# Optimization experiments

Measured on AMD Instinct MI355X. Metric: run time of the kernel, lower is better.

## Reference

```python
import jax, jax.numpy as jnp
import numpy as np

N_NODES = 50000
N_EDGES = 800000
IN_DIM = 128
HIDDEN = 128
CLASSES = 64


def setup_inputs() -> dict:
    key = jax.random.key(0)
    ks = jax.random.split(key, 10)
    features = jax.random.normal(ks[0], (N_NODES, IN_DIM), dtype=jnp.float32)
    W1 = jax.random.normal(ks[1], (HIDDEN, IN_DIM), dtype=jnp.float32) * (2.0 / np.sqrt(IN_DIM + HIDDEN))
    b1 = jnp.zeros((HIDDEN,), dtype=jnp.float32)
    W2 = jax.random.normal(ks[2], (CLASSES, HIDDEN), dtype=jnp.float32) * (2.0 / np.sqrt(HIDDEN + CLASSES))
    b2 = jnp.zeros((CLASSES,), dtype=jnp.float32)
    order_attn = jax.random.uniform(ks[3], (2,), dtype=jnp.float32)
    src1 = jax.random.randint(ks[4], (N_EDGES,), 0, N_NODES, dtype=jnp.int32)
    dst1 = jax.random.randint(ks[5], (N_EDGES,), 0, N_NODES, dtype=jnp.int32)
    src2 = jax.random.randint(ks[6], (N_EDGES,), 0, N_NODES, dtype=jnp.int32)
    dst2 = jax.random.randint(ks[7], (N_EDGES,), 0, N_NODES, dtype=jnp.int32)
    return {"features": features, "W1": W1, "b1": b1, "W2": W2, "b2": b2,
            "order_attn": order_attn, "src1": src1, "dst1": dst1,
            "src2": src2, "dst2": dst2}


def _gin_conv(x, src, dst, W, b):
    # DGL GINConv, aggregator_type='sum', eps=0 (default, non-learnable):
    # h_v = Linear( x_v + sum_{(u->v) in E} x_u )
    agg = jax.ops.segment_sum(x[src], dst, num_segments=N_NODES)  # [N, D]
    return (x + agg) @ W.T + b


def reference(features, W1, b1, W2, b2, order_attn, src1, dst1, src2, dst2):
    a0, a1 = order_attn[0], order_attn[1]
    # layer 1 over both order-graphs
    x11 = jax.nn.elu(a0 * _gin_conv(features, src1, dst1, W1, b1))
    x12 = jax.nn.elu(a1 * _gin_conv(features, src2, dst2, W1, b1))
    x1 = x11 + x12  # [N, hidden]
    # layer 2 over both order-graphs
    x21 = jax.nn.elu(a0 * _gin_conv(x1, src1, dst1, W2, b2))
    x22 = jax.nn.elu(a1 * _gin_conv(x1, src2, dst2, W2, b2))
    return x21 + x22  # [N, classes]
```

## Files before the change

kernel.cpp:

```cpp
#include <hip/hip_runtime.h>
#include <math.h>

#define N_NODES 50000
#define N_EDGES 800000
#define IN_DIM 128
#define HIDDEN 128
#define CLASSES 64
#define N2 100000

#define BIN_SHIFT 8
#define BIN_SZ 256
#define NB 391
#define NBLK 256
#define CHUNK ((2 * N_EDGES + NBLK - 1) / NBLK)

#define NSTRIP 3125
#define GBLK 391

typedef __attribute__((ext_vector_type(8))) short bf16x8;
typedef __attribute__((ext_vector_type(4))) float f32x4;

union FragU {
    uint4 u4;
    uint2 u2[2];
    bf16x8 f;
};

static __device__ __forceinline__ float elu_f(float x) {
    return x > 0.f ? x : (expf(x) - 1.f);
}

static __device__ __forceinline__ unsigned pack_bf2(float a, float b) {
    unsigned ua = __float_as_uint(a);
    ua = (ua + 0x7FFFu + ((ua >> 16) & 1u)) >> 16;
    unsigned ub = __float_as_uint(b);
    ub = (ub + 0x7FFFu + ((ub >> 16) & 1u)) >> 16;
    return ua | (ub << 16);
}

static __device__ __forceinline__ unsigned short bf1(float x) {
    unsigned u = __float_as_uint(x);
    u = (u + 0x7FFFu + ((u >> 16) & 1u)) >> 16;
    return (unsigned short)u;
}

static __device__ __forceinline__ float2 bf2f2(unsigned u) {
    float2 r;
    r.x = __uint_as_float(u << 16);
    r.y = __uint_as_float(u & 0xFFFF0000u);
    return r;
}

static __device__ __forceinline__ void acc4(float4& a, const uint2 u) {
    const float2 lo = bf2f2(u.x);
    const float2 hi = bf2f2(u.y);
    a.x += lo.x; a.y += lo.y; a.z += hi.x; a.w += hi.y;
}

__global__ __launch_bounds__(1024) void k_p1_count(
    const int* __restrict__ dst1, const int* __restrict__ dst2,
    int* __restrict__ counts)
{
    __shared__ int hist[NB];
    const int t = threadIdx.x, b = blockIdx.x;
    if (t < NB) hist[t] = 0;
    __syncthreads();
    const int beg = b * CHUNK;
    const int end = min(beg + CHUNK, 2 * N_EDGES);
    for (int i = beg + t; i < end; i += 1024) {
        const int idx = (i < N_EDGES) ? dst1[i] : (N_NODES + dst2[i - N_EDGES]);
        atomicAdd(&hist[idx >> BIN_SHIFT], 1);
    }
    __syncthreads();
    if (t < NB) counts[t * NBLK + b] = hist[t];
}

__global__ __launch_bounds__(512) void k_scan_bins(
    int* __restrict__ counts, int* __restrict__ binStart, int* __restrict__ off)
{
    __shared__ int tot[512];
    const int t = threadIdx.x;
    int total = 0;
    if (t < NB) {
        const int4* p = reinterpret_cast<const int4*>(counts + t * NBLK);
        #pragma unroll 8
        for (int i = 0; i < NBLK / 4; ++i) {
            const int4 c = p[i];
            total += (c.x + c.y) + (c.z + c.w);
        }
    }
    tot[t] = (t < NB) ? total : 0;
    __syncthreads();
    const int v = tot[t];
    for (int d = 1; d < 512; d <<= 1) {
        const int x = (t >= d) ? tot[t - d] : 0;
        __syncthreads();
        tot[t] += x;
        __syncthreads();
    }
    const int excl = tot[t] - v;
    if (t < NB) binStart[t] = excl;
    if (t == NB - 1) binStart[NB] = tot[t];
    if (t == 0) off[N2] = 2 * N_EDGES;
    if (t < NB) {
        int run = excl;
        int* p = counts + t * NBLK;
        for (int i = 0; i < NBLK; i += 4) {
            int4 c = *reinterpret_cast<int4*>(p + i);
            int4 w;
            w.x = run; run += c.x;
            w.y = run; run += c.y;
            w.z = run; run += c.z;
            w.w = run; run += c.w;
            *reinterpret_cast<int4*>(p + i) = w;
        }
    }
}

__global__ __launch_bounds__(1024) void k_p2_scatter(
    const int* __restrict__ src1, const int* __restrict__ dst1,
    const int* __restrict__ src2, const int* __restrict__ dst2,
    const int* __restrict__ counts, unsigned* __restrict__ binned)
{
    __shared__ int cur[NB];
    const int t = threadIdx.x, b = blockIdx.x;
    if (t < NB) cur[t] = counts[t * NBLK + b];
    __syncthreads();
    const int beg = b * CHUNK;
    const int end = min(beg + CHUNK, 2 * N_EDGES);
    for (int i = beg + t; i < end; i += 1024) {
        int s, idx;
        if (i < N_EDGES) { s = src1[i]; idx = dst1[i]; }
        else             { s = src2[i - N_EDGES]; idx = N_NODES + dst2[i - N_EDGES]; }
        const int bin = idx >> BIN_SHIFT;
        const unsigned rec = ((unsigned)s << BIN_SHIFT) | (unsigned)(idx & (BIN_SZ - 1));
        const int pos = atomicAdd(&cur[bin], 1);
        binned[pos] = rec;
    }
}

__global__ __launch_bounds__(1024) void k_p3_csr(
    const unsigned* __restrict__ binned, const int* __restrict__ binStart,
    int* __restrict__ off, int* __restrict__ csr)
{
    __shared__ int hist[BIN_SZ], sc[BIN_SZ], cur[BIN_SZ];
    const int t = threadIdx.x, bin = blockIdx.x;
    const int bs = binStart[bin], be = binStart[bin + 1];
    const int base = bin << BIN_SHIFT;
    const int nloc = min(BIN_SZ, N2 - base);
    if (t < BIN_SZ) hist[t] = 0;
    __syncthreads();
    for (int p = bs + t; p < be; p += 1024)
        atomicAdd(&hist[binned[p] & (BIN_SZ - 1u)], 1);
    __syncthreads();
    int v = 0;
    if (t < BIN_SZ) { v = hist[t]; sc[t] = v; }
    __syncthreads();
    for (int d = 1; d < BIN_SZ; d <<= 1) {
        int x = 0;
        if (t < BIN_SZ && t >= d) x = sc[t - d];
        __syncthreads();
        if (t < BIN_SZ) sc[t] += x;
        __syncthreads();
    }
    if (t < BIN_SZ) {
        const int excl = sc[t] - v;
        cur[t] = bs + excl;
        if (t < nloc) off[base + t] = bs + excl;
    }
    __syncthreads();
    for (int p = bs + t; p < be; p += 1024) {
        const unsigned rec = binned[p];
        const int pos = atomicAdd(&cur[rec & (BIN_SZ - 1u)], 1);
        csr[pos] = (int)(rec >> BIN_SHIFT);
    }
}

__global__ __launch_bounds__(256) void k_gemm1(
    const float* __restrict__ f, const float* __restrict__ W1,
    unsigned short* __restrict__ y1q)
{
    __shared__ unsigned short Wl[HIDDEN][140];
    const int t = threadIdx.x;
    for (int i = t * 4; i < HIDDEN * IN_DIM; i += 1024) {
        const float4 w = *reinterpret_cast<const float4*>(W1 + i);
        const int o = i >> 7, k = i & 127;
        uint2 p;
        p.x = pack_bf2(w.x, w.y);
        p.y = pack_bf2(w.z, w.w);
        *reinterpret_cast<uint2*>(&Wl[o][k]) = p;
    }
    __syncthreads();

    const int wv = t >> 6;
    const int l  = t & 63;
    const int rc = l & 15;
    const int kq = l >> 4;

    const int sid0 = (blockIdx.x * 4 + wv) * 2;
    const int sid1 = sid0 + 1;
    const bool v0 = sid0 < NSTRIP, v1 = sid1 < NSTRIP;
    const int m0 = min(sid0, NSTRIP - 1) * 16;
    const int m1 = min(sid1, NSTRIP - 1) * 16;

    f32x4 acc[2][8];
    #pragma unroll
    for (int st = 0; st < 2; ++st)
        #pragma unroll
        for (int nt = 0; nt < 8; ++nt)
            acc[st][nt] = (f32x4){0.f, 0.f, 0.f, 0.f};

    #pragma unroll
    for (int kc = 0; kc < 4; ++kc) {
        const int kbase = kc * 32 + kq * 8;
        const float* ap0 = f + (size_t)(m0 + rc) * IN_DIM + kbase;
        const float* ap1 = f + (size_t)(m1 + rc) * IN_DIM + kbase;
        const float4 fa0 = *reinterpret_cast<const float4*>(ap0);
        const float4 fa1 = *reinterpret_cast<const float4*>(ap0 + 4);
        const float4 fb0 = *reinterpret_cast<const float4*>(ap1);
        const float4 fb1 = *reinterpret_cast<const float4*>(ap1 + 4);
        FragU A0, A1;
        A0.u4.x = pack_bf2(fa0.x, fa0.y); A0.u4.y = pack_bf2(fa0.z, fa0.w);
        A0.u4.z = pack_bf2(fa1.x, fa1.y); A0.u4.w = pack_bf2(fa1.z, fa1.w);
        A1.u4.x = pack_bf2(fb0.x, fb0.y); A1.u4.y = pack_bf2(fb0.z, fb0.w);
        A1.u4.z = pack_bf2(fb1.x, fb1.y); A1.u4.w = pack_bf2(fb1.z, fb1.w);
        #pragma unroll
        for (int nt = 0; nt < 8; ++nt) {
            const unsigned short* bp = &Wl[nt * 16 + rc][kbase];
            FragU B;
            B.u2[0] = *reinterpret_cast<const uint2*>(bp);
            B.u2[1] = *reinterpret_cast<const uint2*>(bp + 4);
            acc[0][nt] = __builtin_amdgcn_mfma_f32_16x16x32_bf16(A0.f, B.f, acc[0][nt], 0, 0, 0);
            acc[1][nt] = __builtin_amdgcn_mfma_f32_16x16x32_bf16(A1.f, B.f, acc[1][nt], 0, 0, 0);
        }
    }

    #pragma unroll
    for (int st = 0; st < 2; ++st) {
        if (st == 0 ? !v0 : !v1) continue;
        const int mb = (st == 0 ? m0 : m1) + (l >> 4) * 4;
        #pragma unroll
        for (int nt = 0; nt < 8; ++nt) {
            const int q = nt >> 1;
            const int dd = (nt & 1) * 16 + rc;
            #pragma unroll
            for (int r = 0; r < 4; ++r) {
                y1q[(((size_t)q * N_NODES + (mb + r)) << 5) + dd] = bf1(acc[st][nt][r]);
            }
        }
    }
}

__global__ __launch_bounds__(256) void k_gemm2(
    const float* __restrict__ x1, const float* __restrict__ W2,
    unsigned short* __restrict__ y2h)
{
    __shared__ unsigned short Wl[CLASSES][140];
    const int t = threadIdx.x;
    for (int i = t * 4; i < CLASSES * IN_DIM; i += 1024) {
        const float4 w = *reinterpret_cast<const float4*>(W2 + i);
        const int o = i >> 7, k = i & 127;
        uint2 p;
        p.x = pack_bf2(w.x, w.y);
        p.y = pack_bf2(w.z, w.w);
        *reinterpret_cast<uint2*>(&Wl[o][k]) = p;
    }
    __syncthreads();

    const int wv = t >> 6;
    const int l  = t & 63;
    const int rc = l & 15;
    const int kq = l >> 4;

    const int sid0 = (blockIdx.x * 4 + wv) * 2;
    const int sid1 = sid0 + 1;
    const bool v0 = sid0 < NSTRIP, v1 = sid1 < NSTRIP;
    const int m0 = min(sid0, NSTRIP - 1) * 16;
    const int m1 = min(sid1, NSTRIP - 1) * 16;

    f32x4 acc[2][4];
    #pragma unroll
    for (int st = 0; st < 2; ++st)
        #pragma unroll
        for (int nt = 0; nt < 4; ++nt)
            acc[st][nt] = (f32x4){0.f, 0.f, 0.f, 0.f};

    #pragma unroll
    for (int kc = 0; kc < 4; ++kc) {
        const int kbase = kc * 32 + kq * 8;
        const float* ap0 = x1 + (size_t)(m0 + rc) * IN_DIM + kbase;
        const float* ap1 = x1 + (size_t)(m1 + rc) * IN_DIM + kbase;
        const float4 fa0 = *reinterpret_cast<const float4*>(ap0);
        const float4 fa1 = *reinterpret_cast<const float4*>(ap0 + 4);
        const float4 fb0 = *reinterpret_cast<const float4*>(ap1);
        const float4 fb1 = *reinterpret_cast<const float4*>(ap1 + 4);
        FragU A0, A1;
        A0.u4.x = pack_bf2(fa0.x, fa0.y); A0.u4.y = pack_bf2(fa0.z, fa0.w);
        A0.u4.z = pack_bf2(fa1.x, fa1.y); A0.u4.w = pack_bf2(fa1.z, fa1.w);
        A1.u4.x = pack_bf2(fb0.x, fb0.y); A1.u4.y = pack_bf2(fb0.z, fb0.w);
        A1.u4.z = pack_bf2(fb1.x, fb1.y); A1.u4.w = pack_bf2(fb1.z, fb1.w);
        #pragma unroll
        for (int nt = 0; nt < 4; ++nt) {
            const unsigned short* bp = &Wl[nt * 16 + rc][kbase];
            FragU B;
            B.u2[0] = *reinterpret_cast<const uint2*>(bp);
            B.u2[1] = *reinterpret_cast<const uint2*>(bp + 4);
            acc[0][nt] = __builtin_amdgcn_mfma_f32_16x16x32_bf16(A0.f, B.f, acc[0][nt], 0, 0, 0);
            acc[1][nt] = __builtin_amdgcn_mfma_f32_16x16x32_bf16(A1.f, B.f, acc[1][nt], 0, 0, 0);
        }
    }

    #pragma unroll
    for (int st = 0; st < 2; ++st) {
        if (st == 0 ? !v0 : !v1) continue;
        const int mb = (st == 0 ? m0 : m1) + (l >> 4) * 4;
        #pragma unroll
        for (int nt = 0; nt < 4; ++nt) {
            const int h = nt >> 1;
            const int dd = (nt & 1) * 16 + rc;
            #pragma unroll
            for (int r = 0; r < 4; ++r) {
                y2h[(((size_t)h * N_NODES + (mb + r)) << 5) + dd] = bf1(acc[st][nt][r]);
            }
        }
    }
}

__global__ __launch_bounds__(256) void k_pull1(
    const unsigned short* __restrict__ y1q,
    const int* __restrict__ off, const int* __restrict__ csr,
    const float* __restrict__ b1, const float* __restrict__ attn,
    float* __restrict__ x1)
{
    const int bid = blockIdx.x;
    const int q = (bid & 7) >> 1;
    const int nb = (bid >> 3) * 2 + (bid & 1);
    const int t = threadIdx.x;
    const int lane = t & 63;
    const int grp = lane >> 3;
    const int c4 = (lane & 7) * 4;
    const int v = nb * 32 + (t >> 6) * 8 + grp;
    if (v >= N_NODES) return;
    const size_t qbase = (size_t)q * N_NODES;

    float4 tot1 = {0.f, 0.f, 0.f, 0.f}, tot2 = {0.f, 0.f, 0.f, 0.f};
    #pragma unroll
    for (int g = 0; g < 2; ++g) {
        const int idx = g * N_NODES + v;
        const int beg = off[idx], end_ = off[idx + 1];
        float4 acc = {0.f, 0.f, 0.f, 0.f};
        int j = beg;
        for (; j + 4 <= end_; j += 4) {
            const int s0 = csr[j], s1 = csr[j + 1], s2 = csr[j + 2], s3 = csr[j + 3];
            const uint2 u0 = *reinterpret_cast<const uint2*>(y1q + (((qbase + s0) << 5) + c4));
            const uint2 u1 = *reinterpret_cast<const uint2*>(y1q + (((qbase + s1) << 5) + c4));
            const uint2 u2 = *reinterpret_cast<const uint2*>(y1q + (((qbase + s2) << 5) + c4));
            const uint2 u3 = *reinterpret_cast<const uint2*>(y1q + (((qbase + s3) << 5) + c4));
            acc4(acc, u0); acc4(acc, u1); acc4(acc, u2); acc4(acc, u3);
        }
        for (; j < end_; ++j) {
            const int s = csr[j];
            const uint2 u = *reinterpret_cast<const uint2*>(y1q + (((qbase + s) << 5) + c4));
            acc4(acc, u);
        }
        if (g == 0) tot1 = acc; else tot2 = acc;
    }

    const uint2 uy = *reinterpret_cast<const uint2*>(y1q + (((qbase + v) << 5) + c4));
    const float2 ylo = bf2f2(uy.x), yhi = bf2f2(uy.y);
    const float4 bb = *reinterpret_cast<const float4*>(b1 + q * 32 + c4);
    const float a0 = attn[0], a1 = attn[1];
    float4 r;
    r.x = elu_f(a0 * (ylo.x + tot1.x + bb.x)) + elu_f(a1 * (ylo.x + tot2.x + bb.x));
    r.y = elu_f(a0 * (ylo.y + tot1.y + bb.y)) + elu_f(a1 * (ylo.y + tot2.y + bb.y));
    r.z = elu_f(a0 * (yhi.x + tot1.z + bb.z)) + elu_f(a1 * (yhi.x + tot2.z + bb.z));
    r.w = elu_f(a0 * (yhi.y + tot1.w + bb.w)) + elu_f(a1 * (yhi.y + tot2.w + bb.w));
    *reinterpret_cast<float4*>(x1 + (size_t)v * HIDDEN + q * 32 + c4) = r;
}

__global__ __launch_bounds__(256) void k_pull2(
    const unsigned short* __restrict__ y2h,
    const int* __restrict__ off, const int* __restrict__ csr,
    const float* __restrict__ b2, const float* __restrict__ attn,
    float* __restrict__ out)
{
    const int bid = blockIdx.x;
    const int h = (bid & 7) >> 2;
    const int nb = (bid >> 3) * 4 + (bid & 3);
    const int t = threadIdx.x;
    const int lane = t & 63;
    const int grp = lane >> 3;
    const int c4 = (lane & 7) * 4;
    const int v = nb * 32 + (t >> 6) * 8 + grp;
    if (v >= N_NODES) return;
    const size_t hbase = (size_t)h * N_NODES;

    float4 tot1 = {0.f, 0.f, 0.f, 0.f}, tot2 = {0.f, 0.f, 0.f, 0.f};
    #pragma unroll
    for (int g = 0; g < 2; ++g) {
        const int idx = g * N_NODES + v;
        const int beg = off[idx], end_ = off[idx + 1];
        float4 acc = {0.f, 0.f, 0.f, 0.f};
        int j = beg;
        for (; j + 4 <= end_; j += 4) {
            const int s0 = csr[j], s1 = csr[j + 1], s2 = csr[j + 2], s3 = csr[j + 3];
            const uint2 u0 = *reinterpret_cast<const uint2*>(y2h + (((hbase + s0) << 5) + c4));
            const uint2 u1 = *reinterpret_cast<const uint2*>(y2h + (((hbase + s1) << 5) + c4));
            const uint2 u2 = *reinterpret_cast<const uint2*>(y2h + (((hbase + s2) << 5) + c4));
            const uint2 u3 = *reinterpret_cast<const uint2*>(y2h + (((hbase + s3) << 5) + c4));
            acc4(acc, u0); acc4(acc, u1); acc4(acc, u2); acc4(acc, u3);
        }
        for (; j < end_; ++j) {
            const int s = csr[j];
            const uint2 u = *reinterpret_cast<const uint2*>(y2h + (((hbase + s) << 5) + c4));
            acc4(acc, u);
        }
        if (g == 0) tot1 = acc; else tot2 = acc;
    }

    const uint2 uy = *reinterpret_cast<const uint2*>(y2h + (((hbase + v) << 5) + c4));
    const float2 ylo = bf2f2(uy.x), yhi = bf2f2(uy.y);
    const float4 bb = *reinterpret_cast<const float4*>(b2 + h * 32 + c4);
    const float a0 = attn[0], a1 = attn[1];
    float4 r;
    r.x = elu_f(a0 * (ylo.x + tot1.x + bb.x)) + elu_f(a1 * (ylo.x + tot2.x + bb.x));
    r.y = elu_f(a0 * (ylo.y + tot1.y + bb.y)) + elu_f(a1 * (ylo.y + tot2.y + bb.y));
    r.z = elu_f(a0 * (yhi.x + tot1.z + bb.z)) + elu_f(a1 * (yhi.x + tot2.z + bb.z));
    r.w = elu_f(a0 * (yhi.y + tot1.w + bb.w)) + elu_f(a1 * (yhi.y + tot2.w + bb.w));
    *reinterpret_cast<float4*>(out + (size_t)v * CLASSES + h * 32 + c4) = r;
}

extern "C" void kernel_launch(void* const* d_in, const int* in_sizes, int n_in,
                              void* d_out, int out_size, void* d_ws, size_t ws_size,
                              hipStream_t stream)
{
    const float* features = (const float*)d_in[0];
    const float* W1   = (const float*)d_in[1];
    const float* b1   = (const float*)d_in[2];
    const float* W2   = (const float*)d_in[3];
    const float* b2   = (const float*)d_in[4];
    const float* attn = (const float*)d_in[5];
    const int* src1   = (const int*)d_in[6];
    const int* dst1   = (const int*)d_in[7];
    const int* src2   = (const int*)d_in[8];
    const int* dst2   = (const int*)d_in[9];
    float* out = (float*)d_out;

    float* x1 = (float*)d_ws;
    unsigned short* y1q = (unsigned short*)(x1 + (size_t)N_NODES * HIDDEN);
    unsigned short* y2h = y1q + (size_t)N_NODES * HIDDEN;
    int* off      = (int*)(y2h + (size_t)N_NODES * CLASSES);
    int* binStart = off + (N2 + 4);
    int* counts   = binStart + 392;
    unsigned* binned = (unsigned*)(counts + NB * NBLK);
    int* csr      = (int*)(binned + 2 * N_EDGES);

    k_p1_count  <<<NBLK, 1024, 0, stream>>>(dst1, dst2, counts);
    k_scan_bins <<<1, 512, 0, stream>>>(counts, binStart, off);
    k_p2_scatter<<<NBLK, 1024, 0, stream>>>(src1, dst1, src2, dst2, counts, binned);
    k_p3_csr    <<<NB, 1024, 0, stream>>>(binned, binStart, off, csr);

    k_gemm1<<<GBLK, 256, 0, stream>>>(features, W1, y1q);
    k_pull1<<<6256, 256, 0, stream>>>(y1q, off, csr, b1, attn, x1);

    k_gemm2<<<GBLK, 256, 0, stream>>>(x1, W2, y2h);
    k_pull2<<<3128, 256, 0, stream>>>(y2h, off, csr, b2, attn, out);
}
```

Baseline: 276.3 us.

## Store GEMM outputs as fp32 16-column slices and deepen pull unrolling

The GEMM outputs are now stored as fp32 in 16-column slabs instead of bf16 32-column slabs. The pull kernels gather one float4 per lane, with 4 lanes per node and 16 nodes per wave, and their neighbour loop is unrolled to 8. This removes the bf16 rounding and unpacking and may improve accuracy, but it doubles the bytes gathered per edge. The binned scratch buffer now aliases the y1s region to save workspace, which is safe only because binning finishes before gemm1 writes y1s.

```diff
diff --git a/kernel.cpp b/kernel.cpp
--- a/kernel.cpp
+++ b/kernel.cpp
@@ -38,23 +38,8 @@
     return ua | (ub << 16);
 }
 
-static __device__ __forceinline__ unsigned short bf1(float x) {
-    unsigned u = __float_as_uint(x);
-    u = (u + 0x7FFFu + ((u >> 16) & 1u)) >> 16;
-    return (unsigned short)u;
-}
-
-static __device__ __forceinline__ float2 bf2f2(unsigned u) {
-    float2 r;
-    r.x = __uint_as_float(u << 16);
-    r.y = __uint_as_float(u & 0xFFFF0000u);
-    return r;
-}
-
-static __device__ __forceinline__ void acc4(float4& a, const uint2 u) {
-    const float2 lo = bf2f2(u.x);
-    const float2 hi = bf2f2(u.y);
-    a.x += lo.x; a.y += lo.y; a.z += hi.x; a.w += hi.y;
+static __device__ __forceinline__ void addf4(float4& a, const float4 b) {
+    a.x += b.x; a.y += b.y; a.z += b.z; a.w += b.w;
 }
 
 __global__ __launch_bounds__(1024) void k_p1_count(
@@ -178,7 +163,7 @@
 
 __global__ __launch_bounds__(256) void k_gemm1(
     const float* __restrict__ f, const float* __restrict__ W1,
-    unsigned short* __restrict__ y1q)
+    float* __restrict__ y1s)
 {
     __shared__ unsigned short Wl[HIDDEN][140];
     const int t = threadIdx.x;
@@ -241,11 +226,9 @@
         const int mb = (st == 0 ? m0 : m1) + (l >> 4) * 4;
         #pragma unroll
         for (int nt = 0; nt < 8; ++nt) {
-            const int q = nt >> 1;
-            const int dd = (nt & 1) * 16 + rc;
             #pragma unroll
             for (int r = 0; r < 4; ++r) {
-                y1q[(((size_t)q * N_NODES + (mb + r)) << 5) + dd] = bf1(acc[st][nt][r]);
+                y1s[(((size_t)nt * N_NODES + (mb + r)) << 4) + rc] = acc[st][nt][r];
             }
         }
     }
@@ -253,7 +236,7 @@
 
 __global__ __launch_bounds__(256) void k_gemm2(
     const float* __restrict__ x1, const float* __restrict__ W2,
-    unsigned short* __restrict__ y2h)
+    float* __restrict__ y2s)
 {
     __shared__ unsigned short Wl[CLASSES][140];
     const int t = threadIdx.x;
@@ -316,32 +299,30 @@
         const int mb = (st == 0 ? m0 : m1) + (l >> 4) * 4;
         #pragma unroll
         for (int nt = 0; nt < 4; ++nt) {
-            const int h = nt >> 1;
-            const int dd = (nt & 1) * 16 + rc;
             #pragma unroll
             for (int r = 0; r < 4; ++r) {
-                y2h[(((size_t)h * N_NODES + (mb + r)) << 5) + dd] = bf1(acc[st][nt][r]);
+                y2s[(((size_t)nt * N_NODES + (mb + r)) << 4) + rc] = acc[st][nt][r];
             }
         }
     }
 }
 
 __global__ __launch_bounds__(256) void k_pull1(
-    const unsigned short* __restrict__ y1q,
+    const float* __restrict__ y1s,
     const int* __restrict__ off, const int* __restrict__ csr,
     const float* __restrict__ b1, const float* __restrict__ attn,
     float* __restrict__ x1)
 {
     const int bid = blockIdx.x;
-    const int q = (bid & 7) >> 1;
-    const int nb = (bid >> 3) * 2 + (bid & 1);
+    const int sl = bid & 7;
+    const int nb = bid >> 3;
     const int t = threadIdx.x;
     const int lane = t & 63;
-    const int grp = lane >> 3;
-    const int c4 = (lane & 7) * 4;
-    const int v = nb * 32 + (t >> 6) * 8 + grp;
+    const int grp = lane >> 2;
+    const int c4 = (lane & 3) * 4;
+    const int v = nb * 64 + (t >> 6) * 16 + grp;
     if (v >= N_NODES) return;
-    const size_t qbase = (size_t)q * N_NODES;
+    const float* yb = y1s + ((size_t)sl * N_NODES << 4);
 
     float4 tot1 = {0.f, 0.f, 0.f, 0.f}, tot2 = {0.f, 0.f, 0.f, 0.f};
     #pragma unroll
@@ -350,50 +331,57 @@
         const int beg = off[idx], end_ = off[idx + 1];
         float4 acc = {0.f, 0.f, 0.f, 0.f};
         int j = beg;
-        for (; j + 4 <= end_; j += 4) {
-            const int s0 = csr[j], s1 = csr[j + 1], s2 = csr[j + 2], s3 = csr[j + 3];
-            const uint2 u0 = *reinterpret_cast<const uint2*>(y1q + (((qbase + s0) << 5) + c4));
-            const uint2 u1 = *reinterpret_cast<const uint2*>(y1q + (((qbase + s1) << 5) + c4));
-            const uint2 u2 = *reinterpret_cast<const uint2*>(y1q + (((qbase + s2) << 5) + c4));
-            const uint2 u3 = *reinterpret_cast<const uint2*>(y1q + (((qbase + s3) << 5) + c4));
-            acc4(acc, u0); acc4(acc, u1); acc4(acc, u2); acc4(acc, u3);
+        for (; j + 8 <= end_; j += 8) {
+            const int s0 = csr[j],     s1 = csr[j + 1];
+            const int s2 = csr[j + 2], s3 = csr[j + 3];
+            const int s4 = csr[j + 4], s5 = csr[j + 5];
+            const int s6 = csr[j + 6], s7 = csr[j + 7];
+            const float4 u0 = *reinterpret_cast<const float4*>(yb + ((s0 << 4) + c4));
+            const float4 u1 = *reinterpret_cast<const float4*>(yb + ((s1 << 4) + c4));
+            const float4 u2 = *reinterpret_cast<const float4*>(yb + ((s2 << 4) + c4));
+            const float4 u3 = *reinterpret_cast<const float4*>(yb + ((s3 << 4) + c4));
+            const float4 u4 = *reinterpret_cast<const float4*>(yb + ((s4 << 4) + c4));
+            const float4 u5 = *reinterpret_cast<const float4*>(yb + ((s5 << 4) + c4));
+            const float4 u6 = *reinterpret_cast<const float4*>(yb + ((s6 << 4) + c4));
+            const float4 u7 = *reinterpret_cast<const float4*>(yb + ((s7 << 4) + c4));
+            addf4(acc, u0); addf4(acc, u1); addf4(acc, u2); addf4(acc, u3);
+            addf4(acc, u4); addf4(acc, u5); addf4(acc, u6); addf4(acc, u7);
         }
         for (; j < end_; ++j) {
             const int s = csr[j];
-            const uint2 u = *reinterpret_cast<const uint2*>(y1q + (((qbase + s) << 5) + c4));
-            acc4(acc, u);
+            const float4 u = *reinterpret_cast<const float4*>(yb + ((s << 4) + c4));
+            addf4(acc, u);
         }
         if (g == 0) tot1 = acc; else tot2 = acc;
     }
 
-    const uint2 uy = *reinterpret_cast<const uint2*>(y1q + (((qbase + v) << 5) + c4));
-    const float2 ylo = bf2f2(uy.x), yhi = bf2f2(uy.y);
-    const float4 bb = *reinterpret_cast<const float4*>(b1 + q * 32 + c4);
+    const float4 yv = *reinterpret_cast<const float4*>(yb + ((v << 4) + c4));
+    const float4 bb = *reinterpret_cast<const float4*>(b1 + sl * 16 + c4);
     const float a0 = attn[0], a1 = attn[1];
     float4 r;
-    r.x = elu_f(a0 * (ylo.x + tot1.x + bb.x)) + elu_f(a1 * (ylo.x + tot2.x + bb.x));
-    r.y = elu_f(a0 * (ylo.y + tot1.y + bb.y)) + elu_f(a1 * (ylo.y + tot2.y + bb.y));
-    r.z = elu_f(a0 * (yhi.x + tot1.z + bb.z)) + elu_f(a1 * (yhi.x + tot2.z + bb.z));
-    r.w = elu_f(a0 * (yhi.y + tot1.w + bb.w)) + elu_f(a1 * (yhi.y + tot2.w + bb.w));
-    *reinterpret_cast<float4*>(x1 + (size_t)v * HIDDEN + q * 32 + c4) = r;
+    r.x = elu_f(a0 * (yv.x + tot1.x + bb.x)) + elu_f(a1 * (yv.x + tot2.x + bb.x));
+    r.y = elu_f(a0 * (yv.y + tot1.y + bb.y)) + elu_f(a1 * (yv.y + tot2.y + bb.y));
+    r.z = elu_f(a0 * (yv.z + tot1.z + bb.z)) + elu_f(a1 * (yv.z + tot2.z + bb.z));
+    r.w = elu_f(a0 * (yv.w + tot1.w + bb.w)) + elu_f(a1 * (yv.w + tot2.w + bb.w));
+    *reinterpret_cast<float4*>(x1 + (size_t)v * HIDDEN + sl * 16 + c4) = r;
 }
 
 __global__ __launch_bounds__(256) void k_pull2(
-    const unsigned short* __restrict__ y2h,
+    const float* __restrict__ y2s,
     const int* __restrict__ off, const int* __restrict__ csr,
     const float* __restrict__ b2, const float* __restrict__ attn,
     float* __restrict__ out)
 {
     const int bid = blockIdx.x;
-    const int h = (bid & 7) >> 2;
-    const int nb = (bid >> 3) * 4 + (bid & 3);
+    const int sl = (bid & 7) >> 1;
+    const int nb = (bid >> 3) * 2 + (bid & 1);
     const int t = threadIdx.x;
     const int lane = t & 63;
-    const int grp = lane >> 3;
-    const int c4 = (lane & 7) * 4;
-    const int v = nb * 32 + (t >> 6) * 8 + grp;
+    const int grp = lane >> 2;
+    const int c4 = (lane & 3) * 4;
+    const int v = nb * 64 + (t >> 6) * 16 + grp;
     if (v >= N_NODES) return;
-    const size_t hbase = (size_t)h * N_NODES;
+    const float* yb = y2s + ((size_t)sl * N_NODES << 4);
 
     float4 tot1 = {0.f, 0.f, 0.f, 0.f}, tot2 = {0.f, 0.f, 0.f, 0.f};
     #pragma unroll
@@ -402,32 +390,39 @@
         const int beg = off[idx], end_ = off[idx + 1];
         float4 acc = {0.f, 0.f, 0.f, 0.f};
         int j = beg;
-        for (; j + 4 <= end_; j += 4) {
-            const int s0 = csr[j], s1 = csr[j + 1], s2 = csr[j + 2], s3 = csr[j + 3];
-            const uint2 u0 = *reinterpret_cast<const uint2*>(y2h + (((hbase + s0) << 5) + c4));
-            const uint2 u1 = *reinterpret_cast<const uint2*>(y2h + (((hbase + s1) << 5) + c4));
-            const uint2 u2 = *reinterpret_cast<const uint2*>(y2h + (((hbase + s2) << 5) + c4));
-            const uint2 u3 = *reinterpret_cast<const uint2*>(y2h + (((hbase + s3) << 5) + c4));
-            acc4(acc, u0); acc4(acc, u1); acc4(acc, u2); acc4(acc, u3);
+        for (; j + 8 <= end_; j += 8) {
+            const int s0 = csr[j],     s1 = csr[j + 1];
+            const int s2 = csr[j + 2], s3 = csr[j + 3];
+            const int s4 = csr[j + 4], s5 = csr[j + 5];
+            const int s6 = csr[j + 6], s7 = csr[j + 7];
+            const float4 u0 = *reinterpret_cast<const float4*>(yb + ((s0 << 4) + c4));
+            const float4 u1 = *reinterpret_cast<const float4*>(yb + ((s1 << 4) + c4));
+            const float4 u2 = *reinterpret_cast<const float4*>(yb + ((s2 << 4) + c4));
+            const float4 u3 = *reinterpret_cast<const float4*>(yb + ((s3 << 4) + c4));
+            const float4 u4 = *reinterpret_cast<const float4*>(yb + ((s4 << 4) + c4));
+            const float4 u5 = *reinterpret_cast<const float4*>(yb + ((s5 << 4) + c4));
+            const float4 u6 = *reinterpret_cast<const float4*>(yb + ((s6 << 4) + c4));
+            const float4 u7 = *reinterpret_cast<const float4*>(yb + ((s7 << 4) + c4));
+            addf4(acc, u0); addf4(acc, u1); addf4(acc, u2); addf4(acc, u3);
+            addf4(acc, u4); addf4(acc, u5); addf4(acc, u6); addf4(acc, u7);
         }
         for (; j < end_; ++j) {
             const int s = csr[j];
-            const uint2 u = *reinterpret_cast<const uint2*>(y2h + (((hbase + s) << 5) + c4));
-            acc4(acc, u);
+            const float4 u = *reinterpret_cast<const float4*>(yb + ((s << 4) + c4));
+            addf4(acc, u);
         }
         if (g == 0) tot1 = acc; else tot2 = acc;
     }
 
-    const uint2 uy = *reinterpret_cast<const uint2*>(y2h + (((hbase + v) << 5) + c4));
-    const float2 ylo = bf2f2(uy.x), yhi = bf2f2(uy.y);
-    const float4 bb = *reinterpret_cast<const float4*>(b2 + h * 32 + c4);
+    const float4 yv = *reinterpret_cast<const float4*>(yb + ((v << 4) + c4));
+    const float4 bb = *reinterpret_cast<const float4*>(b2 + sl * 16 + c4);
     const float a0 = attn[0], a1 = attn[1];
     float4 r;
-    r.x = elu_f(a0 * (ylo.x + tot1.x + bb.x)) + elu_f(a1 * (ylo.x + tot2.x + bb.x));
-    r.y = elu_f(a0 * (ylo.y + tot1.y + bb.y)) + elu_f(a1 * (ylo.y + tot2.y + bb.y));
-    r.z = elu_f(a0 * (yhi.x + tot1.z + bb.z)) + elu_f(a1 * (yhi.x + tot2.z + bb.z));
-    r.w = elu_f(a0 * (yhi.y + tot1.w + bb.w)) + elu_f(a1 * (yhi.y + tot2.w + bb.w));
-    *reinterpret_cast<float4*>(out + (size_t)v * CLASSES + h * 32 + c4) = r;
+    r.x = elu_f(a0 * (yv.x + tot1.x + bb.x)) + elu_f(a1 * (yv.x + tot2.x + bb.x));
+    r.y = elu_f(a0 * (yv.y + tot1.y + bb.y)) + elu_f(a1 * (yv.y + tot2.y + bb.y));
+    r.z = elu_f(a0 * (yv.z + tot1.z + bb.z)) + elu_f(a1 * (yv.z + tot2.z + bb.z));
+    r.w = elu_f(a0 * (yv.w + tot1.w + bb.w)) + elu_f(a1 * (yv.w + tot2.w + bb.w));
+    *reinterpret_cast<float4*>(out + (size_t)v * CLASSES + sl * 16 + c4) = r;
 }
 
 extern "C" void kernel_launch(void* const* d_in, const int* in_sizes, int n_in,
@@ -446,23 +441,23 @@
     const int* dst2   = (const int*)d_in[9];
     float* out = (float*)d_out;
 
-    float* x1 = (float*)d_ws;
-    unsigned short* y1q = (unsigned short*)(x1 + (size_t)N_NODES * HIDDEN);
-    unsigned short* y2h = y1q + (size_t)N_NODES * HIDDEN;
-    int* off      = (int*)(y2h + (size_t)N_NODES * CLASSES);
+    float* x1  = (float*)d_ws;
+    float* y1s = x1 + (size_t)N_NODES * HIDDEN;
+    float* y2s = y1s + (size_t)N_NODES * HIDDEN;
+    int* off      = (int*)(y2s + (size_t)N_NODES * CLASSES);
     int* binStart = off + (N2 + 4);
     int* counts   = binStart + 392;
-    unsigned* binned = (unsigned*)(counts + NB * NBLK);
-    int* csr      = (int*)(binned + 2 * N_EDGES);
+    int* csr      = counts + NB * NBLK;
+    unsigned* binned = (unsigned*)y1s;
 
     k_p1_count  <<<NBLK, 1024, 0, stream>>>(dst1, dst2, counts);
     k_scan_bins <<<1, 512, 0, stream>>>(counts, binStart, off);
     k_p2_scatter<<<NBLK, 1024, 0, stream>>>(src1, dst1, src2, dst2, counts, binned);
     k_p3_csr    <<<NB, 1024, 0, stream>>>(binned, binStart, off, csr);
 
-    k_gemm1<<<GBLK, 256, 0, stream>>>(features, W1, y1q);
-    k_pull1<<<6256, 256, 0, stream>>>(y1q, off, csr, b1, attn, x1);
-
-    k_gemm2<<<GBLK, 256, 0, stream>>>(x1, W2, y2h);
-    k_pull2<<<3128, 256, 0, stream>>>(y2h, off, csr, b2, attn, out);
-}
+    k_gemm1<<<GBLK, 256, 0, stream>>>(features, W1, y1s);
+    k_pull1<<<6256, 256, 0, stream>>>(y1s, off, csr, b1, attn, x1);
+
+    k_gemm2<<<GBLK, 256, 0, stream>>>(x1, W2, y2s);
+    k_pull2<<<3128, 256, 0, stream>>>(y2s, off, csr, b2, attn, out);
+}
```

New measurement: 319.5 us. +15.7%, slower.
